# Kernel tuning notes

Hardware: AMD Instinct MI355X
Metric: run time of the kernel (lower is better)

Reference implementation:

```python
import jax, jax.numpy as jnp
import numpy as np

N_SRC, N_DST, E = 200000, 100000, 400000
IN, H, D = 128, 8, 32
F_U, F_I, F_E = 300, 200, 64
LN_EPS = 1e-5


def _seg_softmax(logits, seg, n):
    # edge_softmax: stable softmax over edges grouped by destination node
    m = jax.ops.segment_max(logits, seg, num_segments=n)
    m = jnp.where(jnp.isfinite(m), m, 0.0)
    z = jnp.exp(logits - m[seg])
    s = jax.ops.segment_sum(z, seg, num_segments=n)
    return z / s[seg]


def setup_inputs():
    key = jax.random.key(0)
    ks = jax.random.split(key, 32)
    r = lambda i, shape, s=1.0: s * jax.random.normal(ks[i], shape, dtype=jnp.float32)
    return {
        'x_user': r(0, (N_SRC, F_U)),
        'x_item': r(1, (N_DST, F_I)),
        'node_emb_user': r(2, (N_SRC, IN)),
        'edge_emb': r(3, (IN,)),
        'edge_feats': r(4, (E, F_E)),
        'src_idx': jax.random.randint(ks[5], (E,), 0, N_SRC),
        'dst_idx': jax.random.randint(ks[6], (E,), 0, N_DST),
        # node/edge feature input linears (normal init, std=0.01 in original)
        'W_nf_user': r(7, (IN, F_U), 0.01), 'b_nf_user': jnp.zeros((IN,), jnp.float32),
        'W_nf_item': r(8, (IN, F_I), 0.01), 'b_nf_item': jnp.zeros((IN,), jnp.float32),
        'W_ef': r(9, (IN, F_E), 0.01), 'b_ef': jnp.zeros((IN,), jnp.float32),
        'W_eattn': r(10, (H, IN), 0.01), 'b_eattn': jnp.zeros((H,), jnp.float32),
        'W_merge': r(11, (H, 2 * H), 0.01), 'b_merge': jnp.zeros((H,), jnp.float32),
        # per-type Q/K/V: in_dim -> out_dim*num_heads
        'W_q_item': r(12, (H * D, IN), 0.02), 'b_q_item': jnp.zeros((H * D,), jnp.float32),
        'W_k_user': r(13, (H * D, IN), 0.02), 'b_k_user': jnp.zeros((H * D,), jnp.float32),
        'W_v_user': r(14, (H * D, IN), 0.02), 'b_v_user': jnp.zeros((H * D,), jnp.float32),
        # node_attn_weight: Linear(out_dim, 1, bias=False) per ntype
        'W_na_user': r(15, (D,), 0.02),
        'W_na_item': r(16, (D,), 0.02),
        'ln_gamma': jnp.ones((H * D,), jnp.float32),
        'ln_beta': jnp.zeros((H * D,), jnp.float32),
    }


def reference(x_user, x_item, node_emb_user, edge_emb, edge_feats, src_idx, dst_idx,
              W_nf_user, b_nf_user, W_nf_item, b_nf_item, W_ef, b_ef,
              W_eattn, b_eattn, W_merge, b_merge,
              W_q_item, b_q_item, W_k_user, b_k_user, W_v_user, b_v_user,
              W_na_user, W_na_item, ln_gamma, ln_beta):
    # per-type input projections (+ type-level edge embedding, per-node src embedding)
    dst_feat = x_item @ W_nf_item.T + b_nf_item + edge_emb                      # [N_dst, IN]
    src_feat = x_user @ W_nf_user.T + b_nf_user + node_emb_user + edge_emb     # [N_src, IN]
    ef = edge_feats @ W_ef.T + b_ef                                            # [E, IN]
    # u_add_e -> edge_softmax over dst groups -> edge attention head logits
    h_add = src_feat[src_idx] + ef                                             # [E, IN]
    temp = _seg_softmax(h_add, dst_idx, N_DST)
    temp_attn = temp @ W_eattn.T + b_eattn                                     # [E, H]
    # per-type Q/K/V
    q = (dst_feat @ W_q_item.T + b_q_item).reshape(N_DST, H, D)
    k = (src_feat @ W_k_user.T + b_k_user).reshape(N_SRC, H, D)
    v = (src_feat @ W_v_user.T + b_v_user).reshape(N_SRC, H, D)
    aq = jnp.einsum('nhd,d->nh', q, W_na_item)                                 # [N_dst, H]
    ak = jnp.einsum('nhd,d->nh', k, W_na_user)                                 # [N_src, H]
    # u_add_v scores, scaled, segment softmax per destination
    logits = (ak[src_idx] + aq[dst_idx]) / jnp.sqrt(jnp.float32(D))            # [E, H]
    self_attn = _seg_softmax(logits, dst_idx, N_DST)
    # attn_merge == 'linear': concat(self_attn, temp_attn) -> H
    merged = jnp.concatenate([self_attn, temp_attn], axis=1) @ W_merge.T + b_merge  # [E, H]
    # weighted value scatter-aggregation to destination nodes
    msg = v[src_idx] * merged[:, :, None]                                      # [E, H, D]
    agg = jax.ops.segment_sum(msg, dst_idx, num_segments=N_DST).reshape(N_DST, H * D)
    # layer norm over H*D
    mu = jnp.mean(agg, axis=-1, keepdims=True)
    var = jnp.var(agg, axis=-1, keepdims=True)
    return (agg - mu) * jax.lax.rsqrt(var + LN_EPS) * ln_gamma + ln_beta
```

## Files before the change

kernel.cpp:

```cpp
#include <hip/hip_runtime.h>
#include <hip/hip_fp16.h>
#include <math.h>
#include <stdio.h>
#include <stdint.h>

#define N_SRC 200000
#define N_DST 100000
#define NE    400000

#define SCAN_CHUNK 1024
#define NSCAN ((N_DST + SCAN_CHUNK - 1) / SCAN_CHUNK)

typedef short bf16x8 __attribute__((ext_vector_type(8)));
typedef float f32x4 __attribute__((ext_vector_type(4)));

__device__ __forceinline__ float bflo(unsigned int u) { return __uint_as_float(u << 16); }
__device__ __forceinline__ float bfhi(unsigned int u) { return __uint_as_float(u & 0xFFFF0000u); }
__device__ __forceinline__ unsigned short f2bf(float f) {
    unsigned int u = __float_as_uint(f);
    u += 0x7FFFu + ((u >> 16) & 1u);
    return (unsigned short)(u >> 16);
}
__device__ __forceinline__ unsigned int packbf(float f0, float f1) {
    return __builtin_amdgcn_perm(__float_as_uint(f1), __float_as_uint(f0), 0x07060302u);
}
__device__ __forceinline__ unsigned char f2e5(float f) {
    __half h = __float2half(f);
    unsigned short b = *reinterpret_cast<unsigned short*>(&h);
    b = (unsigned short)(b + 0x7Fu + ((b >> 8) & 1u));
    return (unsigned char)(b >> 8);
}
__device__ __forceinline__ float e52f(unsigned int b8) {
    unsigned short h = (unsigned short)(b8 << 8);
    __half hh = *reinterpret_cast<__half*>(&h);
    return __half2float(hh);
}
__device__ __forceinline__ void gl2lds(const void* g, void* l) {
    __builtin_amdgcn_global_load_lds(
        (const __attribute__((address_space(1))) unsigned int*)g,
        (__attribute__((address_space(3))) unsigned int*)l, 16, 0, 0);
}

template<int K, int KP, int NT, bool FUSEV, bool DOT>
__global__ __launch_bounds__(256) void gemm_fused(
    const float* __restrict__ Ap, const unsigned short* __restrict__ Wf,
    const float* __restrict__ bias, const float* __restrict__ add_n,
    const float* __restrict__ add_c,
    unsigned short* __restrict__ out_lin, unsigned char* __restrict__ out_exp,
    const unsigned short* __restrict__ wvfrag, const float* __restrict__ bv,
    unsigned short* __restrict__ vout,
    const unsigned short* __restrict__ dotfrag, float* __restrict__ dotout,
    int N, int C)
{
    constexpr int KST = KP / 32;
    __shared__ __align__(16) char LDSB[49152];
    char* As = LDSB;
    char* Bs = LDSB + 32768;
    char* T  = LDSB;

    const int tid  = threadIdx.x;
    const int lane = tid & 63;
    const int wv   = tid >> 6;
    const int fr   = lane & 15;
    const int fq   = lane >> 4;
    const int row0 = blockIdx.y * 128;
    const int NTC  = C / 16;

    f32x4 acc[2][NT];
#pragma unroll
    for (int m = 0; m < 2; ++m)
#pragma unroll
        for (int n = 0; n < NT; ++n) acc[m][n] = (f32x4){0.f, 0.f, 0.f, 0.f};

    const int csw = (lane & 7) ^ (lane >> 3);

    auto stage = [&](int buf, int ks) {
        char* ab = As + buf * 16384;
        char* bb = Bs + buf * 8192;
        const char* Af = (const char*)Ap;
#pragma unroll
        for (int q = 0; q < 4; ++q) {
            int i   = wv * 4 + q;
            int row = i * 8 + (lane >> 3);
            int rr  = row0 + row; if (rr >= N) rr = N - 1;
            int kk  = ks * 32 + csw * 4;
            long off = (long)rr * K + ((kk + 4 <= K) ? kk : 0);
            gl2lds(Af + off * 4, ab + i * 1024 + lane * 16);
        }
        const char* wbase = (const char*)Wf + ((size_t)ks * NTC) * 1024;
#pragma unroll
        for (int q = 0; q < 2; ++q) {
            int i = wv * 2 + q;
            gl2lds(wbase + i * 1024 + lane * 16, bb + i * 1024 + lane * 16);
        }
    };

    stage(0, 0);
    for (int ks = 0; ks < KST; ++ks) {
        const int cur = ks & 1;
        if (ks + 1 < KST) {
            stage(cur ^ 1, ks + 1);
            asm volatile("s_waitcnt vmcnt(6)" ::: "memory");
        } else {
            asm volatile("s_waitcnt vmcnt(0)" ::: "memory");
        }
        __builtin_amdgcn_s_barrier();

        const char* ab = As + cur * 16384;
        const char* bb = Bs + cur * 8192;
        const int rA = fr & 7;
        float4 f0 = *(const float4*)(ab + (wv * 32 +      fr) * 128 + ((2 * fq)     ^ rA) * 16);
        float4 f1 = *(const float4*)(ab + (wv * 32 +      fr) * 128 + ((2 * fq + 1) ^ rA) * 16);
        float4 f2 = *(const float4*)(ab + (wv * 32 + 16 + fr) * 128 + ((2 * fq)     ^ rA) * 16);
        float4 f3 = *(const float4*)(ab + (wv * 32 + 16 + fr) * 128 + ((2 * fq + 1) ^ rA) * 16);
        uint4 u0, u1;
        u0.x = packbf(f0.x, f0.y); u0.y = packbf(f0.z, f0.w);
        u0.z = packbf(f1.x, f1.y); u0.w = packbf(f1.z, f1.w);
        u1.x = packbf(f2.x, f2.y); u1.y = packbf(f2.z, f2.w);
        u1.z = packbf(f3.x, f3.y); u1.w = packbf(f3.z, f3.w);
        bf16x8 a0 = *(bf16x8*)&u0;
        bf16x8 a1 = *(bf16x8*)&u1;
        uint4 pb[NT];
#pragma unroll
        for (int n = 0; n < NT; ++n)
            pb[n] = *(const uint4*)(bb + n * 1024 + lane * 16);
#pragma unroll
        for (int n = 0; n < NT; ++n) {
            acc[0][n] = __builtin_amdgcn_mfma_f32_16x16x32_bf16(a0, *(bf16x8*)&pb[n], acc[0][n], 0, 0, 0);
            acc[1][n] = __builtin_amdgcn_mfma_f32_16x16x32_bf16(a1, *(bf16x8*)&pb[n], acc[1][n], 0, 0, 0);
        }
        asm volatile("s_waitcnt lgkmcnt(0)" ::: "memory");
        __builtin_amdgcn_s_barrier();
    }

    float bc[NT];
#pragma unroll
    for (int n = 0; n < NT; ++n) {
        int col = n * 16 + fr;
        float b = 0.f;
        if (bias)  b += bias[col];
        if (add_c) b += add_c[col];
        bc[n] = b;
    }
#pragma unroll
    for (int m = 0; m < 2; ++m) {
#pragma unroll
        for (int j = 0; j < 4; ++j) {
            int rl  = wv * 32 + m * 16 + fq * 4 + j;
            int row = row0 + rl;
            bool rok = (row < N);
#pragma unroll
            for (int n = 0; n < NT; ++n) {
                int col = n * 16 + fr;
                float v = acc[m][n][j] + bc[n];
                if (add_n && rok) v += add_n[(long)row * C + col];
                unsigned short bf = f2bf(v);
                if (FUSEV || DOT) {
                    int c = col >> 3;
                    *(unsigned short*)(T + rl * 256 + ((c ^ (rl & 7)) * 16) + (col & 7) * 2) = bf;
                }
                if (rok) {
                    long o = (long)row * C + col;
                    if (out_lin) out_lin[o] = bf;
                    if (out_exp) out_exp[o] = f2e5(expf(v));
                }
            }
        }
    }

    if (FUSEV || DOT) {
        __syncthreads();
        auto tfrag = [&](int r, int c) -> bf16x8 {
            return *(const bf16x8*)(T + r * 256 + ((c ^ (r & 7)) * 16));
        };
        if (DOT) {
            f32x4 da[2];
            da[0] = (f32x4){0.f, 0.f, 0.f, 0.f};
            da[1] = (f32x4){0.f, 0.f, 0.f, 0.f};
#pragma unroll
            for (int ks = 0; ks < 4; ++ks) {
                bf16x8 bf = *(const bf16x8*)&dotfrag[((size_t)ks * 64 + lane) * 8];
                bf16x8 t0 = tfrag(wv * 32 +      fr, ks * 4 + fq);
                bf16x8 t1 = tfrag(wv * 32 + 16 + fr, ks * 4 + fq);
                da[0] = __builtin_amdgcn_mfma_f32_16x16x32_bf16(t0, bf, da[0], 0, 0, 0);
                da[1] = __builtin_amdgcn_mfma_f32_16x16x32_bf16(t1, bf, da[1], 0, 0, 0);
            }
#pragma unroll
            for (int m = 0; m < 2; ++m)
#pragma unroll
                for (int j = 0; j < 4; ++j) {
                    int row = row0 + wv * 32 + m * 16 + fq * 4 + j;
                    if (fr < 8 && row < N) dotout[(long)row * 8 + fr] = da[m][j];
                }
        }
        if (FUSEV) {
#pragma unroll
            for (int half = 0; half < 2; ++half) {
                f32x4 va[2][8];
#pragma unroll
                for (int m = 0; m < 2; ++m)
#pragma unroll
                    for (int n = 0; n < 8; ++n) va[m][n] = (f32x4){0.f, 0.f, 0.f, 0.f};
#pragma unroll
                for (int ks = 0; ks < 4; ++ks) {
                    bf16x8 t0 = tfrag(wv * 32 +      fr, ks * 4 + fq);
                    bf16x8 t1 = tfrag(wv * 32 + 16 + fr, ks * 4 + fq);
                    uint4 vb4[8];
#pragma unroll
                    for (int n = 0; n < 8; ++n)
                        vb4[n] = *(const uint4*)&wvfrag[(((size_t)ks * 16 + half * 8 + n) * 64 + lane) * 8];
#pragma unroll
                    for (int n = 0; n < 8; ++n) {
                        va[0][n] = __builtin_amdgcn_mfma_f32_16x16x32_bf16(t0, *(bf16x8*)&vb4[n], va[0][n], 0, 0, 0);
                        va[1][n] = __builtin_amdgcn_mfma_f32_16x16x32_bf16(t1, *(bf16x8*)&vb4[n], va[1][n], 0, 0, 0);
                    }
                }
#pragma unroll
                for (int m = 0; m < 2; ++m)
#pragma unroll
                    for (int j = 0; j < 4; ++j) {
                        int row = row0 + wv * 32 + m * 16 + fq * 4 + j;
                        if (row >= N) continue;
#pragma unroll
                        for (int n = 0; n < 8; ++n) {
                            int col = half * 128 + n * 16 + fr;
                            vout[(long)row * 256 + col] = f2bf(va[m][n][j] + bv[col]);
                        }
                    }
            }
        }
    }
}

__global__ void wconv_frag(const float* __restrict__ src, unsigned short* __restrict__ dst,
                           int C, int K, int Kp)
{
    int NTC = C >> 4;
    int total = C * Kp;
    for (int i = blockIdx.x * blockDim.x + threadIdx.x; i < total; i += gridDim.x * blockDim.x) {
        int j  = i & 7;
        int l  = (i >> 3) & 63;
        int t  = i >> 9;
        int n  = t % NTC;
        int ks = t / NTC;
        int col = n * 16 + (l & 15);
        int k   = ks * 32 + ((l >> 4) << 3) + j;
        dst[i] = (k < K) ? f2bf(src[(long)col * K + k]) : (unsigned short)0;
    }
}

__global__ void eff_setup(const float* __restrict__ Wq, const float* __restrict__ bq,
                          const float* __restrict__ na_item,
                          const float* __restrict__ Wk, const float* __restrict__ bk,
                          const float* __restrict__ na_user,
                          const float* __restrict__ W_merge, const float* __restrict__ b_merge,
                          const float* __restrict__ W_eattn, const float* __restrict__ b_eattn,
                          float* __restrict__ wq_eff, float* __restrict__ bq_eff,
                          float* __restrict__ wk_eff, float* __restrict__ bk_eff,
                          float* __restrict__ Wcomb, float* __restrict__ cmv,
                          unsigned short* __restrict__ wqf, unsigned short* __restrict__ wkf)
{
    int tid = threadIdx.x;
    for (int idx = tid; idx < 1024; idx += 256) {
        int h = idx >> 7, k = idx & 127;
        float s1 = 0.f, s2 = 0.f, s3 = 0.f;
        for (int d = 0; d < 32; ++d) {
            s1 += Wq[(h * 32 + d) * 128 + k] * na_item[d];
            s2 += Wk[(h * 32 + d) * 128 + k] * na_user[d];
        }
        for (int j = 0; j < 8; ++j)
            s3 += W_merge[h * 16 + 8 + j] * W_eattn[j * 128 + k];
        wq_eff[idx] = s1;
        wk_eff[idx] = s2;
        Wcomb[idx]  = s3;
    }
    if (tid < 8) {
        float s1 = 0.f, s2 = 0.f, s3 = b_merge[tid];
        for (int d = 0; d < 32; ++d) {
            s1 += bq[tid * 32 + d] * na_item[d];
            s2 += bk[tid * 32 + d] * na_user[d];
        }
        for (int j = 0; j < 8; ++j) s3 += W_merge[tid * 16 + 8 + j] * b_eattn[j];
        bq_eff[tid] = s1;
        bk_eff[tid] = s2;
        cmv[tid]    = s3;
    }
    __syncthreads();
    for (int idx = tid; idx < 2048; idx += 256) {
        int j  = idx & 7;
        int l  = (idx >> 3) & 63;
        int ks = idx >> 9;
        int col = l & 15;
        int k   = ks * 32 + ((l >> 4) << 3) + j;
        wqf[idx] = (col < 8) ? f2bf(wq_eff[col * 128 + k]) : (unsigned short)0;
        wkf[idx] = (col < 8) ? f2bf(wk_eff[col * 128 + k]) : (unsigned short)0;
    }
}

__global__ void hist_kernel(const int* __restrict__ dst_idx, int* __restrict__ cnt)
{
    int e = blockIdx.x * blockDim.x + threadIdx.x;
    if (e < NE) atomicAdd(&cnt[dst_idx[e]], 1);
}

__global__ __launch_bounds__(256) void blocksum_kernel(const int* __restrict__ cnt,
                                                       int* __restrict__ bsum)
{
    __shared__ int sm[256];
    int b = blockIdx.x, t = threadIdx.x;
    int s = 0;
    for (int i = t; i < SCAN_CHUNK; i += 256) {
        int idx = b * SCAN_CHUNK + i;
        if (idx < N_DST) s += cnt[idx];
    }
    sm[t] = s; __syncthreads();
    for (int off = 128; off > 0; off >>= 1) {
        if (t < off) sm[t] += sm[t + off];
        __syncthreads();
    }
    if (t == 0) bsum[b] = sm[0];
}

__global__ void scanoff_kernel(const int* __restrict__ bsum, int* __restrict__ boff)
{
    if (threadIdx.x == 0) {
        int r = 0;
        for (int i = 0; i < NSCAN; ++i) { boff[i] = r; r += bsum[i]; }
    }
}

__global__ __launch_bounds__(256) void rowstart_kernel(
    const int* __restrict__ cnt, const int* __restrict__ boff,
    int* __restrict__ row_start, int* __restrict__ cursor)
{
    __shared__ int sm[256];
    int b = blockIdx.x, t = threadIdx.x;
    int base = b * SCAN_CHUNK + t * 4;
    int c[4]; int tot = 0;
#pragma unroll
    for (int j = 0; j < 4; ++j) {
        int idx = base + j;
        c[j] = (idx < N_DST) ? cnt[idx] : 0;
        tot += c[j];
    }
    sm[t] = tot; __syncthreads();
    for (int off = 1; off < 256; off <<= 1) {
        int v = (t >= off) ? sm[t - off] : 0;
        __syncthreads();
        sm[t] += v;
        __syncthreads();
    }
    int run = sm[t] - tot + boff[b];
#pragma unroll
    for (int j = 0; j < 4; ++j) {
        int idx = base + j;
        if (idx < N_DST) { row_start[idx] = run; cursor[idx] = run; run += c[j]; }
    }
    if (b == 0 && t == 0) row_start[N_DST] = NE;
}

__global__ void scatter_kernel(const int* __restrict__ dst_idx,
                               int* __restrict__ cursor, int* __restrict__ eorder)
{
    int e = blockIdx.x * blockDim.x + threadIdx.x;
    if (e >= NE) return;
    int pos = atomicAdd(&cursor[dst_idx[e]], 1);
    eorder[pos] = e;
}

__global__ __launch_bounds__(256) void fused_gather4(
    const int* __restrict__ row_start, const int* __restrict__ eorder,
    const int* __restrict__ src_idx,
    const unsigned char* __restrict__ Pb, const unsigned char* __restrict__ esfb,
    const unsigned short* __restrict__ vb,
    const float* __restrict__ aq, const float* __restrict__ ak,
    const float* __restrict__ Wcomb, const float* __restrict__ cmv,
    const float* __restrict__ W_merge,
    const float* __restrict__ ln_gamma, const float* __restrict__ ln_beta,
    float* __restrict__ out)
{
    int gw   = (blockIdx.x * blockDim.x + threadIdx.x) >> 6;
    int lane = threadIdx.x & 63;
    if (gw >= N_DST) return;
    const int dst = gw;
    const int r0 = row_start[dst], r1 = row_start[dst + 1];
    const int deg = r1 - r0;
    const int ch = lane * 2;
    const int hl = lane & 7;
    const int g  = lane >> 3;
    const float rsc = 0.17677669529663687f;

    float ax = 0.f, ay = 0.f, az = 0.f, aw = 0.f;

    if (deg > 0) {
        float wc0[8], wc1[8];
#pragma unroll
        for (int h = 0; h < 8; ++h) {
            wc0[h] = Wcomb[h * 128 + ch];
            wc1[h] = Wcomb[h * 128 + ch + 1];
        }
        const float wself = W_merge[g * 16 + hl];
        const float cmg   = cmv[g];
        const float aqh   = aq[(long)dst * 8 + hl];

        if (deg <= 8) {
            int eo[8], sr[8];
            unsigned int pu[8], su[8];
            float akv[8];
            uint2 vv[8];
#pragma unroll
            for (int j = 0; j < 8; ++j) { pu[j] = 0u; su[j] = 0u; akv[j] = 0.f;
                                          vv[j] = make_uint2(0u, 0u); }
#pragma unroll
            for (int j = 0; j < 8; ++j) if (j < deg) eo[j] = eorder[r0 + j];
#pragma unroll
            for (int j = 0; j < 8; ++j) if (j < deg) sr[j] = src_idx[eo[j]];
#pragma unroll
            for (int j = 0; j < 8; ++j) if (j < deg) {
                pu[j]  = *(const unsigned short*)&Pb[(long)eo[j] * 128 + ch];
                su[j]  = *(const unsigned short*)&esfb[(long)sr[j] * 128 + ch];
                akv[j] = ak[(long)sr[j] * 8 + hl];
                vv[j]  = *(const uint2*)&vb[(long)sr[j] * 256 + lane * 4];
            }
            float z0[8], z1[8], ex[8];
            float s1x = 0.f, s1y = 0.f, s2l = 0.f;
#pragma unroll
            for (int j = 0; j < 8; ++j) {
                z0[j] = e52f(pu[j] & 0xFFu) * e52f(su[j] & 0xFFu);
                z1[j] = e52f(pu[j] >> 8)    * e52f(su[j] >> 8);
                s1x += z0[j];
                s1y += z1[j];
                float e = expf((akv[j] + aqh) * rsc);
                ex[j] = (j < deg) ? e : 0.f;
                s2l += ex[j];
            }
            const float i1x = 1.0f / fmaxf(s1x, 1e-35f);
            const float i1y = 1.0f / fmaxf(s1y, 1e-35f);
            const float i2  = 1.0f / s2l;
#pragma unroll
            for (int j = 0; j < 8; ++j) if (j < deg) {
                float t0 = z0[j] * i1x;
                float t1 = z1[j] * i1y;
                float part[8];
#pragma unroll
                for (int h = 0; h < 8; ++h) part[h] = t0 * wc0[h] + t1 * wc1[h];
                int b0 = lane & 1, b1 = (lane >> 1) & 1, b2 = (lane >> 2) & 1;
                float u0 = (b0 ? part[1] : part[0]) + __shfl_xor(b0 ? part[0] : part[1], 1);
                float u1 = (b0 ? part[3] : part[2]) + __shfl_xor(b0 ? part[2] : part[3], 1);
                float u2 = (b0 ? part[5] : part[4]) + __shfl_xor(b0 ? part[4] : part[5], 1);
                float u3 = (b0 ? part[7] : part[6]) + __shfl_xor(b0 ? part[6] : part[7], 1);
                float w0 = (b1 ? u1 : u0) + __shfl_xor(b1 ? u0 : u1, 2);
                float w1 = (b1 ? u3 : u2) + __shfl_xor(b1 ? u2 : u3, 2);
                float ts = (b2 ? w1 : w0) + __shfl_xor(b2 ? w0 : w1, 4);
                ts += __shfl_xor(ts, 8);
                ts += __shfl_xor(ts, 16);
                ts += __shfl_xor(ts, 32);
                float ms = wself * (ex[j] * i2);
                ms += __shfl_xor(ms, 1);
                ms += __shfl_xor(ms, 2);
                ms += __shfl_xor(ms, 4);
                float mm = cmg + ms + __shfl(ts, g);
                ax += mm * bflo(vv[j].x); ay += mm * bfhi(vv[j].x);
                az += mm * bflo(vv[j].y); aw += mm * bfhi(vv[j].y);
            }
        } else {
            float s1x = 0.f, s1y = 0.f, s2l = 0.f;
            for (int j = r0; j < r1; ++j) {
                int eo  = eorder[j];
                int src = src_idx[eo];
                unsigned int pu = *(const unsigned short*)&Pb[(long)eo * 128 + ch];
                unsigned int su = *(const unsigned short*)&esfb[(long)src * 128 + ch];
                float akh = ak[(long)src * 8 + hl];
                s1x += e52f(pu & 0xFFu) * e52f(su & 0xFFu);
                s1y += e52f(pu >> 8)    * e52f(su >> 8);
                s2l += expf((akh + aqh) * rsc);
            }
            const float i1x = 1.0f / fmaxf(s1x, 1e-35f);
            const float i1y = 1.0f / fmaxf(s1y, 1e-35f);
            const float i2  = 1.0f / s2l;
            for (int j = r0; j < r1; ++j) {
                int eo  = eorder[j];
                int src = src_idx[eo];
                unsigned int pu = *(const unsigned short*)&Pb[(long)eo * 128 + ch];
                unsigned int su = *(const unsigned short*)&esfb[(long)src * 128 + ch];
                float akh = ak[(long)src * 8 + hl];
                uint2 vv = *(const uint2*)&vb[(long)src * 256 + lane * 4];
                float t0 = e52f(pu & 0xFFu) * e52f(su & 0xFFu) * i1x;
                float t1 = e52f(pu >> 8)    * e52f(su >> 8)    * i1y;
                float part[8];
#pragma unroll
                for (int h = 0; h < 8; ++h) part[h] = t0 * wc0[h] + t1 * wc1[h];
                int b0 = lane & 1, b1 = (lane >> 1) & 1, b2 = (lane >> 2) & 1;
                float u0 = (b0 ? part[1] : part[0]) + __shfl_xor(b0 ? part[0] : part[1], 1);
                float u1 = (b0 ? part[3] : part[2]) + __shfl_xor(b0 ? part[2] : part[3], 1);
                float u2 = (b0 ? part[5] : part[4]) + __shfl_xor(b0 ? part[4] : part[5], 1);
                float u3 = (b0 ? part[7] : part[6]) + __shfl_xor(b0 ? part[6] : part[7], 1);
                float w0 = (b1 ? u1 : u0) + __shfl_xor(b1 ? u0 : u1, 2);
                float w1 = (b1 ? u3 : u2) + __shfl_xor(b1 ? u2 : u3, 2);
                float ts = (b2 ? w1 : w0) + __shfl_xor(b2 ? w0 : w1, 4);
                ts += __shfl_xor(ts, 8);
                ts += __shfl_xor(ts, 16);
                ts += __shfl_xor(ts, 32);
                float ms = wself * (expf((akh + aqh) * rsc) * i2);
                ms += __shfl_xor(ms, 1);
                ms += __shfl_xor(ms, 2);
                ms += __shfl_xor(ms, 4);
                float mm = cmg + ms + __shfl(ts, g);
                ax += mm * bflo(vv.x); ay += mm * bfhi(vv.x);
                az += mm * bflo(vv.y); aw += mm * bfhi(vv.y);
            }
        }
    }

    float s = ax + ay + az + aw;
    float q = ax * ax + ay * ay + az * az + aw * aw;
#pragma unroll
    for (int off = 32; off > 0; off >>= 1) {
        s += __shfl_xor(s, off);
        q += __shfl_xor(q, off);
    }
    float mu  = s * (1.0f / 256.0f);
    float var = q * (1.0f / 256.0f) - mu * mu;
    float inv = rsqrtf(var + 1e-5f);
    float4 gg = *(const float4*)&ln_gamma[lane * 4];
    float4 bb = *(const float4*)&ln_beta[lane * 4];
    float4 o;
    o.x = (ax - mu) * inv * gg.x + bb.x;
    o.y = (ay - mu) * inv * gg.y + bb.y;
    o.z = (az - mu) * inv * gg.z + bb.z;
    o.w = (aw - mu) * inv * gg.w + bb.w;
    *(float4*)&out[(long)dst * 256 + lane * 4] = o;
}

extern "C" void kernel_launch(void* const* d_in, const int* in_sizes, int n_in,
                              void* d_out, int out_size, void* d_ws, size_t ws_size,
                              hipStream_t stream)
{
    const float* x_user        = (const float*)d_in[0];
    const float* x_item        = (const float*)d_in[1];
    const float* node_emb_user = (const float*)d_in[2];
    const float* edge_emb      = (const float*)d_in[3];
    const float* edge_feats    = (const float*)d_in[4];
    const int*   src_idx       = (const int*)d_in[5];
    const int*   dst_idx       = (const int*)d_in[6];
    const float* W_nf_user     = (const float*)d_in[7];
    const float* b_nf_user     = (const float*)d_in[8];
    const float* W_nf_item     = (const float*)d_in[9];
    const float* b_nf_item     = (const float*)d_in[10];
    const float* W_ef          = (const float*)d_in[11];
    const float* b_ef          = (const float*)d_in[12];
    const float* W_eattn       = (const float*)d_in[13];
    const float* b_eattn       = (const float*)d_in[14];
    const float* W_merge       = (const float*)d_in[15];
    const float* b_merge       = (const float*)d_in[16];
    const float* W_q           = (const float*)d_in[17];
    const float* b_q           = (const float*)d_in[18];
    const float* W_k           = (const float*)d_in[19];
    const float* b_k           = (const float*)d_in[20];
    const float* W_v           = (const float*)d_in[21];
    const float* b_v           = (const float*)d_in[22];
    const float* W_na_user     = (const float*)d_in[23];
    const float* W_na_item     = (const float*)d_in[24];
    const float* ln_gamma      = (const float*)d_in[25];
    const float* ln_beta       = (const float*)d_in[26];

    unsigned char* esf8 = (unsigned char*)d_ws;
    unsigned char* P8   = esf8 + 25600000;
    unsigned short* v_b = (unsigned short*)(P8 + 51200000);
    float* fz     = (float*)(v_b + 51200000);
    float* aq     = fz;
    float* ak     = aq + 800000;
    float* wq_eff = ak + 1600000;
    float* wk_eff = wq_eff + 1024;
    float* bq_eff = wk_eff + 1024;
    float* bk_eff = bq_eff + 16;
    float* Wcomb  = bk_eff + 16;
    float* cmv    = Wcomb + 1024;
    int*   cnt       = (int*)(cmv + 8);
    int*   bsum      = cnt + N_DST;
    int*   boff      = bsum + 128;
    int*   row_start = boff + 128;
    int*   cursor    = row_start + N_DST + 1;
    int*   eorder    = cursor + N_DST;
    unsigned short* wub = (unsigned short*)(((uintptr_t)(eorder + NE) + 15) & ~(uintptr_t)15);
    unsigned short* wib = wub + 128 * 320;
    unsigned short* web = wib + 128 * 224;
    unsigned short* wvb = web + 128 * 64;
    unsigned short* wqf = wvb + 256 * 128;
    unsigned short* wkf = wqf + 2048;
    size_t needed = (size_t)((char*)(wkf + 2048) - (char*)d_ws);
    if (ws_size < needed) {
        fprintf(stderr, "kernel_launch: ws_size %zu < needed %zu\n", ws_size, needed);
        return;
    }

    hipMemsetAsync(cnt, 0, N_DST * sizeof(int), stream);

    eff_setup<<<1, 256, 0, stream>>>(W_q, b_q, W_na_item, W_k, b_k, W_na_user,
                                     W_merge, b_merge, W_eattn, b_eattn,
                                     wq_eff, bq_eff, wk_eff, bk_eff, Wcomb, cmv,
                                     wqf, wkf);

    wconv_frag<<<64, 256, 0, stream>>>(W_nf_user, wub, 128, 300, 320);
    wconv_frag<<<64, 256, 0, stream>>>(W_nf_item, wib, 128, 200, 224);
    wconv_frag<<<32, 256, 0, stream>>>(W_ef,      web, 128,  64,  64);
    wconv_frag<<<64, 256, 0, stream>>>(W_v,       wvb, 256, 128, 128);

    gemm_fused<300, 320, 8, true, true><<<dim3(1, 1563), 256, 0, stream>>>(
        x_user, wub, b_nf_user, node_emb_user, edge_emb,
        nullptr, esf8, wvb, b_v, v_b, wkf, ak, N_SRC, 128);
    gemm_fused<200, 224, 8, false, true><<<dim3(1, 782), 256, 0, stream>>>(
        x_item, wib, b_nf_item, nullptr, edge_emb,
        nullptr, nullptr, nullptr, nullptr, nullptr, wqf, aq, N_DST, 128);
    gemm_fused<64, 64, 8, false, false><<<dim3(1, 3125), 256, 0, stream>>>(
        edge_feats, web, b_ef, nullptr, nullptr,
        nullptr, P8, nullptr, nullptr, nullptr, nullptr, nullptr, NE, 128);

    hist_kernel<<<1563, 256, 0, stream>>>(dst_idx, cnt);
    blocksum_kernel<<<NSCAN, 256, 0, stream>>>(cnt, bsum);
    scanoff_kernel<<<1, 64, 0, stream>>>(bsum, boff);
    rowstart_kernel<<<NSCAN, 256, 0, stream>>>(cnt, boff, row_start, cursor);
    scatter_kernel<<<1563, 256, 0, stream>>>(dst_idx, cursor, eorder);

    fused_gather4<<<25000, 256, 0, stream>>>(
        row_start, eorder, src_idx, P8, esf8, v_b, aq, ak,
        Wcomb, cmv, W_merge, ln_gamma, ln_beta, (float*)d_out);
}
```

Before: 652.3 us.

## Merge three node/edge GEMMs into one launch and read weights from global

Replaces the three separate gemm_fused launches with a single gemm_all kernel whose blocks are interleaved by a 2:1:4 ratio across the user, item and edge GEMMs, so the three workloads share the GPU concurrently and pay fewer launch and tail costs. Weight fragments are now loaded straight from global memory into registers each k-step instead of being staged through LDS, which shrinks shared memory from 48KB to 32KB and should allow higher occupancy. The wait counts are adjusted for the extra in-flight loads. The trade-off is more redundant global or L2 weight reads per block and more register pressure from the mixed template bodies in one kernel.

```diff
diff --git a/kernel.cpp b/kernel.cpp
--- a/kernel.cpp
+++ b/kernel.cpp
@@ -42,7 +42,8 @@
 }
 
 template<int K, int KP, int NT, bool FUSEV, bool DOT>
-__global__ __launch_bounds__(256) void gemm_fused(
+__device__ __forceinline__ void gemm_body(
+    int tileY, char* LDSB,
     const float* __restrict__ Ap, const unsigned short* __restrict__ Wf,
     const float* __restrict__ bias, const float* __restrict__ add_n,
     const float* __restrict__ add_c,
@@ -53,9 +54,7 @@
     int N, int C)
 {
     constexpr int KST = KP / 32;
-    __shared__ __align__(16) char LDSB[49152];
     char* As = LDSB;
-    char* Bs = LDSB + 32768;
     char* T  = LDSB;
 
     const int tid  = threadIdx.x;
@@ -63,7 +62,7 @@
     const int wv   = tid >> 6;
     const int fr   = lane & 15;
     const int fq   = lane >> 4;
-    const int row0 = blockIdx.y * 128;
+    const int row0 = tileY * 128;
     const int NTC  = C / 16;
 
     f32x4 acc[2][NT];
@@ -74,9 +73,8 @@
 
     const int csw = (lane & 7) ^ (lane >> 3);
 
-    auto stage = [&](int buf, int ks) {
+    auto stageA = [&](int buf, int ks) {
         char* ab = As + buf * 16384;
-        char* bb = Bs + buf * 8192;
         const char* Af = (const char*)Ap;
 #pragma unroll
         for (int q = 0; q < 4; ++q) {
@@ -87,27 +85,24 @@
             long off = (long)rr * K + ((kk + 4 <= K) ? kk : 0);
             gl2lds(Af + off * 4, ab + i * 1024 + lane * 16);
         }
-        const char* wbase = (const char*)Wf + ((size_t)ks * NTC) * 1024;
-#pragma unroll
-        for (int q = 0; q < 2; ++q) {
-            int i = wv * 2 + q;
-            gl2lds(wbase + i * 1024 + lane * 16, bb + i * 1024 + lane * 16);
-        }
     };
 
-    stage(0, 0);
+    stageA(0, 0);
     for (int ks = 0; ks < KST; ++ks) {
         const int cur = ks & 1;
+        uint4 pb[NT];
+#pragma unroll
+        for (int n = 0; n < NT; ++n)
+            pb[n] = *(const uint4*)&Wf[(((size_t)ks * NTC + n) * 64 + lane) * 8];
         if (ks + 1 < KST) {
-            stage(cur ^ 1, ks + 1);
-            asm volatile("s_waitcnt vmcnt(6)" ::: "memory");
+            stageA(cur ^ 1, ks + 1);
+            asm volatile("s_waitcnt vmcnt(12)" ::: "memory");
         } else {
-            asm volatile("s_waitcnt vmcnt(0)" ::: "memory");
+            asm volatile("s_waitcnt vmcnt(8)" ::: "memory");
         }
         __builtin_amdgcn_s_barrier();
 
         const char* ab = As + cur * 16384;
-        const char* bb = Bs + cur * 8192;
         const int rA = fr & 7;
         float4 f0 = *(const float4*)(ab + (wv * 32 +      fr) * 128 + ((2 * fq)     ^ rA) * 16);
         float4 f1 = *(const float4*)(ab + (wv * 32 +      fr) * 128 + ((2 * fq + 1) ^ rA) * 16);
@@ -120,10 +115,6 @@
         u1.z = packbf(f3.x, f3.y); u1.w = packbf(f3.z, f3.w);
         bf16x8 a0 = *(bf16x8*)&u0;
         bf16x8 a1 = *(bf16x8*)&u1;
-        uint4 pb[NT];
-#pragma unroll
-        for (int n = 0; n < NT; ++n)
-            pb[n] = *(const uint4*)(bb + n * 1024 + lane * 16);
 #pragma unroll
         for (int n = 0; n < NT; ++n) {
             acc[0][n] = __builtin_amdgcn_mfma_f32_16x16x32_bf16(a0, *(bf16x8*)&pb[n], acc[0][n], 0, 0, 0);
@@ -229,6 +220,43 @@
                     }
             }
         }
+    }
+}
+
+__global__ __launch_bounds__(256) void gemm_all(
+    const float* __restrict__ x_user, const unsigned short* __restrict__ wub,
+    const float* __restrict__ b_nf_user, const float* __restrict__ node_emb_user,
+    const float* __restrict__ edge_emb,
+    unsigned char* __restrict__ esf8,
+    const unsigned short* __restrict__ wvb, const float* __restrict__ bv,
+    unsigned short* __restrict__ v_b,
+    const unsigned short* __restrict__ wkf, float* __restrict__ ak,
+    const float* __restrict__ x_item, const unsigned short* __restrict__ wib,
+    const float* __restrict__ b_nf_item,
+    const unsigned short* __restrict__ wqf, float* __restrict__ aq,
+    const float* __restrict__ edge_feats, const unsigned short* __restrict__ web,
+    const float* __restrict__ b_ef, unsigned char* __restrict__ P8)
+{
+    __shared__ __align__(16) char LDSB[32768];
+    int gid = blockIdx.x;
+    int b = gid / 7;
+    int r = gid - b * 7;
+    if (r < 2) {
+        int t = b * 2 + r;
+        if (t < 1563)
+            gemm_body<300, 320, 8, true, true>(t, LDSB,
+                x_user, wub, b_nf_user, node_emb_user, edge_emb,
+                nullptr, esf8, wvb, bv, v_b, wkf, ak, N_SRC, 128);
+    } else if (r == 2) {
+        gemm_body<200, 224, 8, false, true>(b, LDSB,
+            x_item, wib, b_nf_item, nullptr, edge_emb,
+            nullptr, nullptr, nullptr, nullptr, nullptr, wqf, aq, N_DST, 128);
+    } else {
+        int t = b * 4 + (r - 3);
+        if (t < 3125)
+            gemm_body<64, 64, 8, false, false>(t, LDSB,
+                edge_feats, web, b_ef, nullptr, nullptr,
+                nullptr, P8, nullptr, nullptr, nullptr, nullptr, nullptr, NE, 128);
     }
 }
 
@@ -606,15 +634,11 @@
     wconv_frag<<<32, 256, 0, stream>>>(W_ef,      web, 128,  64,  64);
     wconv_frag<<<64, 256, 0, stream>>>(W_v,       wvb, 256, 128, 128);
 
-    gemm_fused<300, 320, 8, true, true><<<dim3(1, 1563), 256, 0, stream>>>(
+    gemm_all<<<5474, 256, 0, stream>>>(
         x_user, wub, b_nf_user, node_emb_user, edge_emb,
-        nullptr, esf8, wvb, b_v, v_b, wkf, ak, N_SRC, 128);
-    gemm_fused<200, 224, 8, false, true><<<dim3(1, 782), 256, 0, stream>>>(
-        x_item, wib, b_nf_item, nullptr, edge_emb,
-        nullptr, nullptr, nullptr, nullptr, nullptr, wqf, aq, N_DST, 128);
-    gemm_fused<64, 64, 8, false, false><<<dim3(1, 3125), 256, 0, stream>>>(
-        edge_feats, web, b_ef, nullptr, nullptr,
-        nullptr, P8, nullptr, nullptr, nullptr, nullptr, nullptr, NE, 128);
+        esf8, wvb, b_v, v_b, wkf, ak,
+        x_item, wib, b_nf_item, wqf, aq,
+        edge_feats, web, b_ef, P8);
 
     hist_kernel<<<1563, 256, 0, stream>>>(dst_idx, cnt);
     blocksum_kernel<<<NSCAN, 256, 0, stream>>>(cnt, bsum);
```

Result: faster. 589.1 us, median of 2 (-9.7%).
